# Kernel tuning notes

Hardware: AMD Instinct MI355X
Metric: run time of the kernel (lower is better)

The kernel has to match this reference:

```python
import jax, jax.numpy as jnp
import numpy as np

B, S, E, H = 4, 2048, 512, 8
DH = E // H
EPS = 1e-5

def _ln(x, g, b):
    m = jnp.mean(x, axis=-1, keepdims=True)
    v = jnp.var(x, axis=-1, keepdims=True)
    return (x - m) * jax.lax.rsqrt(v + EPS) * g + b

def setup_inputs() -> dict:
    key = jax.random.key(0)
    ks = jax.random.split(key, 8)
    sc = 0.02
    return {
        "x": jax.random.normal(ks[0], (B, S, E), dtype=jnp.float32),
        "ln1_g": jnp.ones((E,), jnp.float32),
        "ln1_b": jnp.zeros((E,), jnp.float32),
        "in_proj_w": sc * jax.random.normal(ks[1], (3 * E, E), jnp.float32),
        "in_proj_b": jnp.zeros((3 * E,), jnp.float32),
        "out_w": sc * jax.random.normal(ks[2], (E, E), jnp.float32),
        "out_b": jnp.zeros((E,), jnp.float32),
        "ln2_g": jnp.ones((E,), jnp.float32),
        "ln2_b": jnp.zeros((E,), jnp.float32),
        "fc1_w": sc * jax.random.normal(ks[3], (E, E), jnp.float32),
        "fc1_b": jnp.zeros((E,), jnp.float32),
        "fc2_w": sc * jax.random.normal(ks[4], (E, E), jnp.float32),
        "fc2_b": jnp.zeros((E,), jnp.float32),
    }

def reference(x, ln1_g, ln1_b, in_proj_w, in_proj_b, out_w, out_b,
              ln2_g, ln2_b, fc1_w, fc1_b, fc2_w, fc2_b):
    # pre-LN
    z = _ln(x, ln1_g, ln1_b)
    # qkv projection (torch MHA packed in_proj: [3E, E])
    qkv = z @ in_proj_w.T + in_proj_b          # [B,S,3E]
    q, k, v = jnp.split(qkv, 3, axis=-1)
    q = q.reshape(B, S, H, DH)
    k = k.reshape(B, S, H, DH)
    v = v.reshape(B, S, H, DH)
    scores = jnp.einsum("bqhd,bkhd->bhqk", q, k) / np.sqrt(DH).astype(np.float32)
    causal = jnp.triu(jnp.ones((S, S), dtype=bool), k=1)  # True = masked
    neg = jnp.finfo(scores.dtype).min
    scores = jnp.where(causal, neg, scores)
    attn = jax.nn.softmax(scores, axis=-1)      # [B,H,S,S]
    ctx = jnp.einsum("bhqk,bkhd->bqhd", attn, v).reshape(B, S, E)
    attn_out = ctx @ out_w.T + out_b
    # torch MHA with need_weights=True averages over heads by default
    attn_weights = jnp.mean(attn, axis=1)       # [B,S,S]
    z2 = x + attn_out
    y = _ln(z2, ln2_g, ln2_b)
    y = jax.nn.leaky_relu(y @ fc1_w.T + fc1_b, negative_slope=0.01)
    y = y @ fc2_w.T + fc2_b
    y = y + z2
    return (y, attn_weights)
```

## Files before the change

kernel.cpp:

```cpp
#include <hip/hip_runtime.h>

typedef short bf16x8 __attribute__((ext_vector_type(8)));
typedef float f32x4 __attribute__((ext_vector_type(4)));
typedef unsigned short u16x8 __attribute__((ext_vector_type(8)));

#define NB 4
#define SQ 2048
#define EM 512
#define NH 8
#define DHD 64
#define QSCALE 0.1803368801111731f

__device__ __forceinline__ unsigned short f2bf(float x) {
  unsigned u = __float_as_uint(x);
  u += 0x7FFFu + ((u >> 16) & 1u);
  return (unsigned short)(u >> 16);
}

__device__ __forceinline__ int sw8(int row, int col8) { return col8 ^ ((row & 7) << 3); }

__device__ __forceinline__ void glds16(const void* g, void* l) {
  __builtin_amdgcn_global_load_lds(
      (const __attribute__((address_space(1))) void*)g,
      (__attribute__((address_space(3))) void*)l, 16, 0, 0);
}

__global__ __launch_bounds__(256) void f2bf4_kernel(
    const float* __restrict__ w0, const float* __restrict__ w1,
    const float* __restrict__ w2, const float* __restrict__ w3,
    unsigned short* __restrict__ o0, unsigned short* __restrict__ o1,
    unsigned short* __restrict__ o2, unsigned short* __restrict__ o3) {
  int i = (blockIdx.x * 256 + threadIdx.x) * 8;
  const float* src;
  unsigned short* dst;
  int off;
  if (i < 786432) { src = w0; dst = o0; off = i; }
  else if (i < 1048576) { src = w1; dst = o1; off = i - 786432; }
  else if (i < 1310720) { src = w2; dst = o2; off = i - 1048576; }
  else { src = w3; dst = o3; off = i - 1310720; }
  f32x4 a = *(const f32x4*)(src + off);
  f32x4 b = *(const f32x4*)(src + off + 4);
  u16x8 o;
#pragma unroll
  for (int j = 0; j < 4; ++j) { o[j] = f2bf(a[j]); o[j + 4] = f2bf(b[j]); }
  *(u16x8*)(dst + off) = o;
}

__global__ __launch_bounds__(256) void ln_kernel(const float* __restrict__ x,
                                                 const float* __restrict__ g,
                                                 const float* __restrict__ bb,
                                                 unsigned short* __restrict__ out) {
  int tid = threadIdx.x;
  int row = blockIdx.x * 4 + (tid >> 6);
  int lane = tid & 63;
  size_t base = (size_t)row * EM + lane * 8;
  f32x4 v0 = *(const f32x4*)(x + base);
  f32x4 v1 = *(const f32x4*)(x + base + 4);
  float s = 0.f, q = 0.f;
#pragma unroll
  for (int j = 0; j < 4; ++j) { s += v0[j] + v1[j]; q += v0[j] * v0[j] + v1[j] * v1[j]; }
#pragma unroll
  for (int m = 1; m < 64; m <<= 1) { s += __shfl_xor(s, m); q += __shfl_xor(q, m); }
  float mean = s * (1.f / EM);
  float var = q * (1.f / EM) - mean * mean;
  float rs = rsqrtf(var + 1e-5f);
  f32x4 g0 = *(const f32x4*)(g + lane * 8), g1 = *(const f32x4*)(g + lane * 8 + 4);
  f32x4 b0 = *(const f32x4*)(bb + lane * 8), b1 = *(const f32x4*)(bb + lane * 8 + 4);
  u16x8 o;
#pragma unroll
  for (int j = 0; j < 4; ++j) {
    o[j] = f2bf((v0[j] - mean) * rs * g0[j] + b0[j]);
    o[j + 4] = f2bf((v1[j] - mean) * rs * g1[j] + b1[j]);
  }
  *(u16x8*)(out + base) = o;
}

template <bool LEAKY, bool RESID, bool OUTF32, bool QKV>
__global__ __launch_bounds__(256) void gemm64(
    const unsigned short* __restrict__ A, const unsigned short* __restrict__ Bm,
    const float* __restrict__ bias, const float* __restrict__ resid,
    float* __restrict__ outf, unsigned short* __restrict__ outh,
    unsigned short* __restrict__ qo, unsigned short* __restrict__ ko,
    unsigned short* __restrict__ vo, int M, int N, int K) {
  __shared__ unsigned short As[2][64][64];
  __shared__ unsigned short Bs[2][64][64];
  int m0 = blockIdx.x * 64, n0 = blockIdx.y * 64;
  int t = threadIdx.x;
  int wv = t >> 6, ln = t & 63, lg = ln >> 4, lr = ln & 15;
  int rsub = ln >> 3;
  int csw = ((ln & 7) ^ rsub) * 8;
  f32x4 acc[4];
#pragma unroll
  for (int c = 0; c < 4; ++c)
#pragma unroll
    for (int r = 0; r < 4; ++r) acc[c][r] = 0.f;

  const unsigned short* ag0 = A + (size_t)(m0 + wv * 16 + rsub) * K + csw;
  const unsigned short* ag1 = A + (size_t)(m0 + wv * 16 + 8 + rsub) * K + csw;
  const unsigned short* bg0 = Bm + (size_t)(n0 + wv * 16 + rsub) * K + csw;
  const unsigned short* bg1 = Bm + (size_t)(n0 + wv * 16 + 8 + rsub) * K + csw;

  glds16(ag0, &As[0][wv * 16][0]);
  glds16(ag1, &As[0][wv * 16 + 8][0]);
  glds16(bg0, &Bs[0][wv * 16][0]);
  glds16(bg1, &Bs[0][wv * 16 + 8][0]);

  int nk = K >> 6;
  for (int ki = 0; ki < nk; ++ki) {
    int cur = ki & 1;
    __syncthreads();
    if (ki + 1 < nk) {
      int nb = cur ^ 1;
      int ko_ = (ki + 1) * 64;
      glds16(ag0 + ko_, &As[nb][wv * 16][0]);
      glds16(ag1 + ko_, &As[nb][wv * 16 + 8][0]);
      glds16(bg0 + ko_, &Bs[nb][wv * 16][0]);
      glds16(bg1 + ko_, &Bs[nb][wv * 16 + 8][0]);
    }
#pragma unroll
    for (int kk = 0; kk < 64; kk += 32) {
      int arw = wv * 16 + lr;
      bf16x8 af = *(const bf16x8*)&As[cur][arw][sw8(arw, kk + lg * 8)];
#pragma unroll
      for (int c = 0; c < 4; ++c) {
        int brw = c * 16 + lr;
        bf16x8 bf = *(const bf16x8*)&Bs[cur][brw][sw8(brw, kk + lg * 8)];
        acc[c] = __builtin_amdgcn_mfma_f32_16x16x32_bf16(af, bf, acc[c], 0, 0, 0);
      }
    }
  }
#pragma unroll
  for (int c = 0; c < 4; ++c) {
    int C_ = n0 + c * 16 + lr;
    float bv = bias[C_];
#pragma unroll
    for (int r = 0; r < 4; ++r) {
      int R_ = m0 + wv * 16 + lg * 4 + r;
      float v = acc[c][r] + bv;
      if (LEAKY) v = v > 0.f ? v : 0.01f * v;
      if (RESID) v += resid[(size_t)R_ * N + C_];
      if (QKV) {
        int which = C_ >> 9, f = C_ & 511, h = f >> 6, d = f & 63;
        int b_ = R_ >> 11, s_ = R_ & 2047;
        if (which == 0) {
          qo[(((size_t)b_ * NH + h) * SQ + s_) * DHD + d] = f2bf(v * QSCALE);
        } else if (which == 1) {
          ko[(((size_t)b_ * NH + h) * SQ + s_) * DHD + d] = f2bf(v);
        } else {
          vo[(((size_t)b_ * NH + h) * DHD + d) * SQ + s_] = f2bf(v);
        }
      } else if (OUTF32) {
        outf[(size_t)R_ * N + C_] = v;
      } else {
        outh[(size_t)R_ * N + C_] = f2bf(v);
      }
    }
  }
}

template <bool QKV>
__global__ __launch_bounds__(256) void gemm128(
    const unsigned short* __restrict__ A, const unsigned short* __restrict__ Bm,
    const float* __restrict__ bias, unsigned short* __restrict__ qo,
    unsigned short* __restrict__ ko, unsigned short* __restrict__ vo,
    int M, int N, int K) {
  __shared__ unsigned short As[2][128][64];
  __shared__ unsigned short Bs[2][128][64];
  int m0 = blockIdx.x * 128, n0 = blockIdx.y * 128;
  int t = threadIdx.x;
  int wv = t >> 6, ln = t & 63, lg = ln >> 4, lr = ln & 15;
  int wr = wv >> 1, wc = wv & 1;
  int rsub = ln >> 3;
  int csw = ((ln & 7) ^ rsub) * 8;
  f32x4 acc[4][4];
#pragma unroll
  for (int m = 0; m < 4; ++m)
#pragma unroll
    for (int n = 0; n < 4; ++n)
#pragma unroll
      for (int r = 0; r < 4; ++r) acc[m][n][r] = 0.f;

  const unsigned short* agb = A + (size_t)(m0 + wv * 8 + rsub) * K + csw;
  const unsigned short* bgb = Bm + (size_t)(n0 + wv * 8 + rsub) * K + csw;

#pragma unroll
  for (int i = 0; i < 4; ++i) {
    glds16(agb + (size_t)(i * 32) * K, &As[0][i * 32 + wv * 8][0]);
    glds16(bgb + (size_t)(i * 32) * K, &Bs[0][i * 32 + wv * 8][0]);
  }

  int nk = K >> 6;
  for (int ki = 0; ki < nk; ++ki) {
    int cur = ki & 1;
    __syncthreads();
    if (ki + 1 < nk) {
      int nb = cur ^ 1;
      int ko_ = (ki + 1) * 64;
#pragma unroll
      for (int i = 0; i < 4; ++i) {
        glds16(agb + (size_t)(i * 32) * K + ko_, &As[nb][i * 32 + wv * 8][0]);
        glds16(bgb + (size_t)(i * 32) * K + ko_, &Bs[nb][i * 32 + wv * 8][0]);
      }
    }
#pragma unroll
    for (int kk = 0; kk < 64; kk += 32) {
      bf16x8 af[4], bfr[4];
#pragma unroll
      for (int m = 0; m < 4; ++m) {
        int arw = wr * 64 + m * 16 + lr;
        af[m] = *(const bf16x8*)&As[cur][arw][sw8(arw, kk + lg * 8)];
      }
#pragma unroll
      for (int n = 0; n < 4; ++n) {
        int brw = wc * 64 + n * 16 + lr;
        bfr[n] = *(const bf16x8*)&Bs[cur][brw][sw8(brw, kk + lg * 8)];
      }
#pragma unroll
      for (int m = 0; m < 4; ++m)
#pragma unroll
        for (int n = 0; n < 4; ++n)
          acc[m][n] = __builtin_amdgcn_mfma_f32_16x16x32_bf16(af[m], bfr[n], acc[m][n], 0, 0, 0);
    }
  }

#pragma unroll
  for (int n = 0; n < 4; ++n) {
    int C_ = n0 + wc * 64 + n * 16 + lr;
    float bv = bias[C_];
#pragma unroll
    for (int m = 0; m < 4; ++m) {
#pragma unroll
      for (int r = 0; r < 4; ++r) {
        int R_ = m0 + wr * 64 + m * 16 + lg * 4 + r;
        float v = acc[m][n][r] + bv;
        int which = C_ >> 9, f = C_ & 511, h = f >> 6, d = f & 63;
        int b_ = R_ >> 11, s_ = R_ & 2047;
        if (which == 0) {
          qo[(((size_t)b_ * NH + h) * SQ + s_) * DHD + d] = f2bf(v * QSCALE);
        } else if (which == 1) {
          ko[(((size_t)b_ * NH + h) * SQ + s_) * DHD + d] = f2bf(v);
        } else {
          vo[(((size_t)b_ * NH + h) * DHD + d) * SQ + s_] = f2bf(v);
        }
      }
    }
  }
}

__global__ __launch_bounds__(256) void flash_kernel(
    const unsigned short* __restrict__ Q, const unsigned short* __restrict__ Kb,
    const unsigned short* __restrict__ Vt, unsigned short* __restrict__ ctx,
    float* __restrict__ mstat, float* __restrict__ lstat) {
  __shared__ unsigned short Ks[2][64][64];
  __shared__ unsigned short Vs[2][64][64];
  __shared__ unsigned short Ps[4][16][64];
  int h = blockIdx.y, b = blockIdx.z;
  int t = threadIdx.x, wv = t >> 6, ln = t & 63, lg = ln >> 4, lr = ln & 15;
  int rsub = ln >> 3;
  int csw = ((ln & 7) ^ rsub) * 8;
  size_t headoff = ((size_t)b * NH + h) * SQ;
  const unsigned short* kg0 = Kb + (headoff + wv * 16 + rsub) * DHD + csw;
  const unsigned short* kg1 = Kb + (headoff + wv * 16 + 8 + rsub) * DHD + csw;
  const unsigned short* vg0 = Vt + (((size_t)b * NH + h) * DHD + wv * 16 + rsub) * SQ + csw;
  const unsigned short* vg1 = Vt + (((size_t)b * NH + h) * DHD + wv * 16 + 8 + rsub) * SQ + csw;

  bf16x8 vones;
#pragma unroll
  for (int j = 0; j < 8; ++j) vones[j] = (lr == 0) ? (short)0x3F80 : (short)0;

  for (int half = 0; half < 2; ++half) {
    int qt = half ? blockIdx.x : (31 - blockIdx.x);
    int qb = qt * 64;
    const unsigned short* qrow = Q + (headoff + qb + wv * 16 + lr) * DHD;
    bf16x8 aq0 = *(const bf16x8*)(qrow + lg * 8);
    bf16x8 aq1 = *(const bf16x8*)(qrow + 32 + lg * 8);

    f32x4 cacc[4], lacc;
#pragma unroll
    for (int nd = 0; nd < 4; ++nd)
#pragma unroll
      for (int r = 0; r < 4; ++r) cacc[nd][r] = 0.f;
#pragma unroll
    for (int r = 0; r < 4; ++r) lacc[r] = 0.f;
    float mrun[4];
#pragma unroll
    for (int r = 0; r < 4; ++r) mrun[r] = -__builtin_inff();

    int nkt = qt + 1;
    __syncthreads();
    glds16(kg0, &Ks[0][wv * 16][0]);
    glds16(kg1, &Ks[0][wv * 16 + 8][0]);
    glds16(vg0, &Vs[0][wv * 16][0]);
    glds16(vg1, &Vs[0][wv * 16 + 8][0]);

    for (int kt = 0; kt < nkt; ++kt) {
      int cur = kt & 1;
      __syncthreads();
      if (kt + 1 < nkt) {
        int nb = cur ^ 1;
        size_t ko_ = (size_t)(kt + 1) * 64;
        glds16(kg0 + ko_ * DHD, &Ks[nb][wv * 16][0]);
        glds16(kg1 + ko_ * DHD, &Ks[nb][wv * 16 + 8][0]);
        glds16(vg0 + ko_, &Vs[nb][wv * 16][0]);
        glds16(vg1 + ko_, &Vs[nb][wv * 16 + 8][0]);
      }

      float sv[4][4];
      __builtin_amdgcn_s_setprio(1);
#pragma unroll
      for (int nt = 0; nt < 4; ++nt) {
        f32x4 sf;
#pragma unroll
        for (int r = 0; r < 4; ++r) sf[r] = 0.f;
        int brw = nt * 16 + lr;
        bf16x8 bk0 = *(const bf16x8*)&Ks[cur][brw][sw8(brw, lg * 8)];
        bf16x8 bk1 = *(const bf16x8*)&Ks[cur][brw][sw8(brw, 32 + lg * 8)];
        sf = __builtin_amdgcn_mfma_f32_16x16x32_bf16(aq0, bk0, sf, 0, 0, 0);
        sf = __builtin_amdgcn_mfma_f32_16x16x32_bf16(aq1, bk1, sf, 0, 0, 0);
#pragma unroll
        for (int r = 0; r < 4; ++r) sv[nt][r] = sf[r];
      }
      __builtin_amdgcn_s_setprio(0);
      if (kt == nkt - 1) {
        int kbase = kt * 64;
#pragma unroll
        for (int nt = 0; nt < 4; ++nt) {
          int kcol = kbase + nt * 16 + lr;
#pragma unroll
          for (int r = 0; r < 4; ++r) {
            int qr = qb + wv * 16 + lg * 4 + r;
            if (kcol > qr) sv[nt][r] = -__builtin_inff();
          }
        }
      }

      float lmax[4];
      bool need = false;
#pragma unroll
      for (int r = 0; r < 4; ++r) {
        lmax[r] = fmaxf(fmaxf(sv[0][r], sv[1][r]), fmaxf(sv[2][r], sv[3][r]));
        need |= (lmax[r] > mrun[r] + 8.f);
      }
      if (__any(need)) {
#pragma unroll
        for (int r = 0; r < 4; ++r) {
          float tm = lmax[r];
#pragma unroll
          for (int m = 1; m < 16; m <<= 1) tm = fmaxf(tm, __shfl_xor(tm, m));
          float mn = fmaxf(mrun[r], tm);
          float sc = exp2f(mrun[r] - mn);
          mrun[r] = mn;
          lacc[r] *= sc;
#pragma unroll
          for (int nd = 0; nd < 4; ++nd) cacc[nd][r] *= sc;
        }
      }
#pragma unroll
      for (int r = 0; r < 4; ++r) {
        int prow = lg * 4 + r;
#pragma unroll
        for (int nt = 0; nt < 4; ++nt) {
          float p = exp2f(sv[nt][r] - mrun[r]);
          Ps[wv][prow][sw8(prow, nt * 16 + lr)] =
              (unsigned short)(__float_as_uint(p) >> 16);
        }
      }

      bf16x8 pf0 = *(const bf16x8*)&Ps[wv][lr][sw8(lr, lg * 8)];
      bf16x8 pf1 = *(const bf16x8*)&Ps[wv][lr][sw8(lr, 32 + lg * 8)];
      __builtin_amdgcn_s_setprio(1);
      lacc = __builtin_amdgcn_mfma_f32_16x16x32_bf16(pf0, vones, lacc, 0, 0, 0);
      lacc = __builtin_amdgcn_mfma_f32_16x16x32_bf16(pf1, vones, lacc, 0, 0, 0);
#pragma unroll
      for (int nd = 0; nd < 4; ++nd) {
        int vrw = nd * 16 + lr;
        bf16x8 vf0 = *(const bf16x8*)&Vs[cur][vrw][sw8(vrw, lg * 8)];
        bf16x8 vf1 = *(const bf16x8*)&Vs[cur][vrw][sw8(vrw, 32 + lg * 8)];
        cacc[nd] = __builtin_amdgcn_mfma_f32_16x16x32_bf16(pf0, vf0, cacc[nd], 0, 0, 0);
        cacc[nd] = __builtin_amdgcn_mfma_f32_16x16x32_bf16(pf1, vf1, cacc[nd], 0, 0, 0);
      }
      __builtin_amdgcn_s_setprio(0);
    }

    float inv[4];
#pragma unroll
    for (int r = 0; r < 4; ++r) inv[r] = 1.f / __shfl(lacc[r], ln & 48);
#pragma unroll
    for (int nd = 0; nd < 4; ++nd)
#pragma unroll
      for (int r = 0; r < 4; ++r) {
        size_t dst = ((size_t)b * SQ + qb + wv * 16 + lg * 4 + r) * EM + h * DHD + nd * 16 + lr;
        ctx[dst] = f2bf(cacc[nd][r] * inv[r]);
      }
    if (lr == 0) {
#pragma unroll
      for (int r = 0; r < 4; ++r) {
        int row = qb + wv * 16 + lg * 4 + r;
        mstat[headoff + row] = mrun[r];
        lstat[headoff + row] = 0.125f * inv[r];
      }
    }
  }
}

__global__ __launch_bounds__(256) void attnw_kernel(
    const unsigned short* __restrict__ Q, const unsigned short* __restrict__ Kb,
    const float* __restrict__ mstat, const float* __restrict__ lstat,
    float* __restrict__ aw) {
  int kt2 = blockIdx.x, qt = blockIdx.y, b = blockIdx.z;
  int qb = qt * 64, kb = kt2 * 128;
  int t = threadIdx.x;
  float* tile = aw + ((size_t)b * SQ + qb) * SQ + kb;
  if (2 * kt2 > qt) {
    int row = t >> 2, cbase = (t & 3) * 32;
    f32x4 z;
#pragma unroll
    for (int j = 0; j < 4; ++j) z[j] = 0.f;
    float* p = tile + (size_t)row * SQ + cbase;
#pragma unroll
    for (int j = 0; j < 8; ++j) *(f32x4*)(p + j * 4) = z;
    return;
  }
  __shared__ unsigned short Ks[2][2][64][64];
  int wv = t >> 6, ln = t & 63, lg = ln >> 4, lr = ln & 15;
  int rsub = ln >> 3;
  int csw = ((ln & 7) ^ rsub) * 8;
  size_t khstride = (size_t)SQ * DHD;
  const unsigned short* kg00 = Kb + (((size_t)b * NH) * SQ + kb + wv * 16 + rsub) * DHD + csw;
  const unsigned short* kg01 = kg00 + (size_t)8 * DHD;
  const unsigned short* kg10 = kg00 + (size_t)64 * DHD;
  const unsigned short* kg11 = kg00 + (size_t)72 * DHD;
  const unsigned short* qg = Q + (((size_t)b * NH) * SQ + qb + wv * 16 + lr) * DHD + lg * 8;
  size_t mbase = (size_t)b * NH * SQ + qb + wv * 16 + lg * 4;

  glds16(kg00, &Ks[0][0][wv * 16][0]);
  glds16(kg01, &Ks[0][0][wv * 16 + 8][0]);
  glds16(kg10, &Ks[0][1][wv * 16][0]);
  glds16(kg11, &Ks[0][1][wv * 16 + 8][0]);

  bf16x8 aqc0 = *(const bf16x8*)qg;
  bf16x8 aqc1 = *(const bf16x8*)(qg + 32);
  bf16x8 aqn0 = *(const bf16x8*)(qg + khstride);
  bf16x8 aqn1 = *(const bf16x8*)(qg + khstride + 32);
  float mmc[4], lic[4], mmn[4], lin[4];
#pragma unroll
  for (int r = 0; r < 4; ++r) {
    mmc[r] = mstat[mbase + r];
    lic[r] = lstat[mbase + r];
    mmn[r] = mstat[mbase + SQ + r];
    lin[r] = lstat[mbase + SQ + r];
  }

  f32x4 facc[2][4];
#pragma unroll
  for (int j = 0; j < 2; ++j)
#pragma unroll
    for (int nt = 0; nt < 4; ++nt)
#pragma unroll
      for (int r = 0; r < 4; ++r) facc[j][nt][r] = 0.f;

  for (int h = 0; h < NH; ++h) {
    int cur = h & 1;
    __syncthreads();
    if (h + 1 < NH) {
      size_t ho = (size_t)(h + 1) * khstride;
      glds16(kg00 + ho, &Ks[cur ^ 1][0][wv * 16][0]);
      glds16(kg01 + ho, &Ks[cur ^ 1][0][wv * 16 + 8][0]);
      glds16(kg10 + ho, &Ks[cur ^ 1][1][wv * 16][0]);
      glds16(kg11 + ho, &Ks[cur ^ 1][1][wv * 16 + 8][0]);
    }

#pragma unroll
    for (int nt = 0; nt < 4; ++nt) {
      int brw = nt * 16 + lr;
      f32x4 sf0, sf1;
#pragma unroll
      for (int r = 0; r < 4; ++r) { sf0[r] = 0.f; sf1[r] = 0.f; }
      bf16x8 bk00 = *(const bf16x8*)&Ks[cur][0][brw][sw8(brw, lg * 8)];
      bf16x8 bk01 = *(const bf16x8*)&Ks[cur][0][brw][sw8(brw, 32 + lg * 8)];
      bf16x8 bk10 = *(const bf16x8*)&Ks[cur][1][brw][sw8(brw, lg * 8)];
      bf16x8 bk11 = *(const bf16x8*)&Ks[cur][1][brw][sw8(brw, 32 + lg * 8)];
      sf0 = __builtin_amdgcn_mfma_f32_16x16x32_bf16(aqc0, bk00, sf0, 0, 0, 0);
      sf1 = __builtin_amdgcn_mfma_f32_16x16x32_bf16(aqc0, bk10, sf1, 0, 0, 0);
      sf0 = __builtin_amdgcn_mfma_f32_16x16x32_bf16(aqc1, bk01, sf0, 0, 0, 0);
      sf1 = __builtin_amdgcn_mfma_f32_16x16x32_bf16(aqc1, bk11, sf1, 0, 0, 0);
#pragma unroll
      for (int r = 0; r < 4; ++r) {
        facc[0][nt][r] += exp2f(sf0[r] - mmc[r]) * lic[r];
        facc[1][nt][r] += exp2f(sf1[r] - mmc[r]) * lic[r];
      }
    }

    aqc0 = aqn0; aqc1 = aqn1;
#pragma unroll
    for (int r = 0; r < 4; ++r) { mmc[r] = mmn[r]; lic[r] = lin[r]; }
    if (h + 2 < NH) {
      aqn0 = *(const bf16x8*)(qg + (size_t)(h + 2) * khstride);
      aqn1 = *(const bf16x8*)(qg + (size_t)(h + 2) * khstride + 32);
#pragma unroll
      for (int r = 0; r < 4; ++r) {
        mmn[r] = mstat[mbase + (size_t)(h + 2) * SQ + r];
        lin[r] = lstat[mbase + (size_t)(h + 2) * SQ + r];
      }
    }
  }

#pragma unroll
  for (int j = 0; j < 2; ++j) {
    int ktj = 2 * kt2 + j;
    bool fullmask = (ktj > qt);
    bool dg = (ktj == qt);
#pragma unroll
    for (int nt = 0; nt < 4; ++nt) {
      int kc = kb + j * 64 + nt * 16 + lr;
#pragma unroll
      for (int r = 0; r < 4; ++r) {
        int qr = qb + wv * 16 + lg * 4 + r;
        float v = (fullmask || (dg && kc > qr)) ? 0.f : facc[j][nt][r];
        tile[(size_t)(wv * 16 + lg * 4 + r) * SQ + j * 64 + nt * 16 + lr] = v;
      }
    }
  }
}

extern "C" void kernel_launch(void* const* d_in, const int* in_sizes, int n_in,
                              void* d_out, int out_size, void* d_ws, size_t ws_size,
                              hipStream_t stream) {
  (void)in_sizes; (void)n_in; (void)out_size; (void)ws_size;
  const float* x = (const float*)d_in[0];
  const float* ln1g = (const float*)d_in[1];
  const float* ln1b = (const float*)d_in[2];
  const float* wqkv = (const float*)d_in[3];
  const float* bqkv = (const float*)d_in[4];
  const float* wout = (const float*)d_in[5];
  const float* bout = (const float*)d_in[6];
  const float* ln2g = (const float*)d_in[7];
  const float* ln2b = (const float*)d_in[8];
  const float* wfc1 = (const float*)d_in[9];
  const float* bfc1 = (const float*)d_in[10];
  const float* wfc2 = (const float*)d_in[11];
  const float* bfc2 = (const float*)d_in[12];

  char* ws = (char*)d_ws;
  unsigned short* zctx = (unsigned short*)(ws);
  unsigned short* qb_ = (unsigned short*)(ws + 8388608);
  unsigned short* kb_ = (unsigned short*)(ws + 16777216);
  unsigned short* vb_ = (unsigned short*)(ws + 25165824);
  float* z2 = (float*)(ws + 33554432);
  float* mstat = (float*)(ws + 50331648);
  float* lstat = (float*)(ws + 50593792);
  unsigned short* wqkv_h = (unsigned short*)(ws + 50855936);
  unsigned short* wout_h = (unsigned short*)(ws + 52428800);
  unsigned short* wfc1_h = (unsigned short*)(ws + 52953088);
  unsigned short* wfc2_h = (unsigned short*)(ws + 53477376);
  unsigned short* y1 = qb_;
  unsigned short* h1 = kb_;

  float* outy = (float*)d_out;
  float* outw = outy + (size_t)NB * SQ * EM;

  f2bf4_kernel<<<768, 256, 0, stream>>>(wqkv, wout, wfc1, wfc2,
                                        wqkv_h, wout_h, wfc1_h, wfc2_h);

  ln_kernel<<<2048, 256, 0, stream>>>(x, ln1g, ln1b, zctx);
  gemm128<true><<<dim3(64, 12), 256, 0, stream>>>(
      zctx, wqkv_h, bqkv, qb_, kb_, vb_, 8192, 1536, 512);
  flash_kernel<<<dim3(16, 8, 4), 256, 0, stream>>>(qb_, kb_, vb_, zctx, mstat, lstat);
  attnw_kernel<<<dim3(16, 32, 4), 256, 0, stream>>>(qb_, kb_, mstat, lstat, outw);
  gemm64<false, true, true, false><<<dim3(128, 8), 256, 0, stream>>>(
      zctx, wout_h, bout, x, z2, nullptr, nullptr, nullptr, nullptr, 8192, 512, 512);
  ln_kernel<<<2048, 256, 0, stream>>>(z2, ln2g, ln2b, y1);
  gemm64<true, false, false, false><<<dim3(128, 8), 256, 0, stream>>>(
      y1, wfc1_h, bfc1, nullptr, nullptr, h1, nullptr, nullptr, nullptr, 8192, 512, 512);
  gemm64<false, true, true, false><<<dim3(128, 8), 256, 0, stream>>>(
      h1, wfc2_h, bfc2, z2, outy, nullptr, nullptr, nullptr, nullptr, 8192, 512, 512);
}
```

Baseline: 186.2 us.

## Widen flash attention key tiles from 64 to 128 keys per iteration

After: 184.8 us. About the same (-0.8%).

```diff
diff --git a/kernel.cpp b/kernel.cpp
--- a/kernel.cpp
+++ b/kernel.cpp
@@ -18,6 +18,7 @@
 }
 
 __device__ __forceinline__ int sw8(int row, int col8) { return col8 ^ ((row & 7) << 3); }
+__device__ __forceinline__ int sw16(int row, int col8) { return col8 ^ ((row & 15) << 3); }
 
 __device__ __forceinline__ void glds16(const void* g, void* l) {
   __builtin_amdgcn_global_load_lds(
@@ -251,18 +252,21 @@
     const unsigned short* __restrict__ Q, const unsigned short* __restrict__ Kb,
     const unsigned short* __restrict__ Vt, unsigned short* __restrict__ ctx,
     float* __restrict__ mstat, float* __restrict__ lstat) {
-  __shared__ unsigned short Ks[2][64][64];
-  __shared__ unsigned short Vs[2][64][64];
-  __shared__ unsigned short Ps[4][16][64];
+  __shared__ unsigned short Ks[2][128][64];
+  __shared__ unsigned short Vs[2][64][128];
+  __shared__ unsigned short Ps[4][16][128];
   int h = blockIdx.y, b = blockIdx.z;
   int t = threadIdx.x, wv = t >> 6, ln = t & 63, lg = ln >> 4, lr = ln & 15;
-  int rsub = ln >> 3;
-  int csw = ((ln & 7) ^ rsub) * 8;
   size_t headoff = ((size_t)b * NH + h) * SQ;
-  const unsigned short* kg0 = Kb + (headoff + wv * 16 + rsub) * DHD + csw;
-  const unsigned short* kg1 = Kb + (headoff + wv * 16 + 8 + rsub) * DHD + csw;
-  const unsigned short* vg0 = Vt + (((size_t)b * NH + h) * DHD + wv * 16 + rsub) * SQ + csw;
-  const unsigned short* vg1 = Vt + (((size_t)b * NH + h) * DHD + wv * 16 + 8 + rsub) * SQ + csw;
+  size_t vbase = ((size_t)b * NH + h) * DHD;
+
+  int cswK = ((ln & 7) ^ (ln >> 3)) * 8;
+  const unsigned short* kgb = Kb + (headoff + wv * 32 + (ln >> 3)) * DHD + cswK;
+  int vrow4 = ln >> 4;
+  const unsigned short* vgb = Vt + (vbase + wv * 16 + vrow4) * SQ;
+  int vcsw[4];
+#pragma unroll
+  for (int g = 0; g < 4; ++g) vcsw[g] = ((ln & 15) ^ (g * 4 + vrow4)) * 8;
 
   bf16x8 vones;
 #pragma unroll
@@ -286,29 +290,32 @@
 #pragma unroll
     for (int r = 0; r < 4; ++r) mrun[r] = -__builtin_inff();
 
-    int nkt = qt + 1;
+    int nkt = (qt + 2) >> 1;
     __syncthreads();
-    glds16(kg0, &Ks[0][wv * 16][0]);
-    glds16(kg1, &Ks[0][wv * 16 + 8][0]);
-    glds16(vg0, &Vs[0][wv * 16][0]);
-    glds16(vg1, &Vs[0][wv * 16 + 8][0]);
+#pragma unroll
+    for (int g = 0; g < 4; ++g) {
+      glds16(kgb + (size_t)(g * 8) * DHD, &Ks[0][wv * 32 + g * 8][0]);
+      glds16(vgb + (size_t)(g * 4) * SQ + vcsw[g], &Vs[0][wv * 16 + g * 4][0]);
+    }
 
     for (int kt = 0; kt < nkt; ++kt) {
       int cur = kt & 1;
+      int kb = kt * 128;
       __syncthreads();
       if (kt + 1 < nkt) {
         int nb = cur ^ 1;
-        size_t ko_ = (size_t)(kt + 1) * 64;
-        glds16(kg0 + ko_ * DHD, &Ks[nb][wv * 16][0]);
-        glds16(kg1 + ko_ * DHD, &Ks[nb][wv * 16 + 8][0]);
-        glds16(vg0 + ko_, &Vs[nb][wv * 16][0]);
-        glds16(vg1 + ko_, &Vs[nb][wv * 16 + 8][0]);
-      }
-
-      float sv[4][4];
+        size_t ko_ = (size_t)(kt + 1) * 128;
+#pragma unroll
+        for (int g = 0; g < 4; ++g) {
+          glds16(kgb + (ko_ + g * 8) * DHD, &Ks[nb][wv * 32 + g * 8][0]);
+          glds16(vgb + (size_t)(g * 4) * SQ + ko_ + vcsw[g], &Vs[nb][wv * 16 + g * 4][0]);
+        }
+      }
+
+      float sv[8][4];
       __builtin_amdgcn_s_setprio(1);
 #pragma unroll
-      for (int nt = 0; nt < 4; ++nt) {
+      for (int nt = 0; nt < 8; ++nt) {
         f32x4 sf;
 #pragma unroll
         for (int r = 0; r < 4; ++r) sf[r] = 0.f;
@@ -322,10 +329,9 @@
       }
       __builtin_amdgcn_s_setprio(0);
       if (kt == nkt - 1) {
-        int kbase = kt * 64;
-#pragma unroll
-        for (int nt = 0; nt < 4; ++nt) {
-          int kcol = kbase + nt * 16 + lr;
+#pragma unroll
+        for (int nt = 0; nt < 8; ++nt) {
+          int kcol = kb + nt * 16 + lr;
 #pragma unroll
           for (int r = 0; r < 4; ++r) {
             int qr = qb + wv * 16 + lg * 4 + r;
@@ -338,7 +344,9 @@
       bool need = false;
 #pragma unroll
       for (int r = 0; r < 4; ++r) {
-        lmax[r] = fmaxf(fmaxf(sv[0][r], sv[1][r]), fmaxf(sv[2][r], sv[3][r]));
+        float m0_ = fmaxf(fmaxf(sv[0][r], sv[1][r]), fmaxf(sv[2][r], sv[3][r]));
+        float m1_ = fmaxf(fmaxf(sv[4][r], sv[5][r]), fmaxf(sv[6][r], sv[7][r]));
+        lmax[r] = fmaxf(m0_, m1_);
         need |= (lmax[r] > mrun[r] + 8.f);
       }
       if (__any(need)) {
@@ -358,26 +366,31 @@
 #pragma unroll
       for (int r = 0; r < 4; ++r) {
         int prow = lg * 4 + r;
-#pragma unroll
-        for (int nt = 0; nt < 4; ++nt) {
+        int rx = (prow & 15) << 3;
+#pragma unroll
+        for (int nt = 0; nt < 8; ++nt) {
           float p = exp2f(sv[nt][r] - mrun[r]);
-          Ps[wv][prow][sw8(prow, nt * 16 + lr)] =
+          Ps[wv][prow][(nt * 16 + lr) ^ rx] =
               (unsigned short)(__float_as_uint(p) >> 16);
         }
       }
 
-      bf16x8 pf0 = *(const bf16x8*)&Ps[wv][lr][sw8(lr, lg * 8)];
-      bf16x8 pf1 = *(const bf16x8*)&Ps[wv][lr][sw8(lr, 32 + lg * 8)];
+      bf16x8 pf[4];
+#pragma unroll
+      for (int ks = 0; ks < 4; ++ks)
+        pf[ks] = *(const bf16x8*)&Ps[wv][lr][sw16(lr, ks * 32 + lg * 8)];
       __builtin_amdgcn_s_setprio(1);
-      lacc = __builtin_amdgcn_mfma_f32_16x16x32_bf16(pf0, vones, lacc, 0, 0, 0);
-      lacc = __builtin_amdgcn_mfma_f32_16x16x32_bf16(pf1, vones, lacc, 0, 0, 0);
+#pragma unroll
+      for (int ks = 0; ks < 4; ++ks)
+        lacc = __builtin_amdgcn_mfma_f32_16x16x32_bf16(pf[ks], vones, lacc, 0, 0, 0);
 #pragma unroll
       for (int nd = 0; nd < 4; ++nd) {
         int vrw = nd * 16 + lr;
-        bf16x8 vf0 = *(const bf16x8*)&Vs[cur][vrw][sw8(vrw, lg * 8)];
-        bf16x8 vf1 = *(const bf16x8*)&Vs[cur][vrw][sw8(vrw, 32 + lg * 8)];
-        cacc[nd] = __builtin_amdgcn_mfma_f32_16x16x32_bf16(pf0, vf0, cacc[nd], 0, 0, 0);
-        cacc[nd] = __builtin_amdgcn_mfma_f32_16x16x32_bf16(pf1, vf1, cacc[nd], 0, 0, 0);
+#pragma unroll
+        for (int ks = 0; ks < 4; ++ks) {
+          bf16x8 vf = *(const bf16x8*)&Vs[cur][vrw][sw16(vrw, ks * 32 + lg * 8)];
+          cacc[nd] = __builtin_amdgcn_mfma_f32_16x16x32_bf16(pf[ks], vf, cacc[nd], 0, 0, 0);
+        }
       }
       __builtin_amdgcn_s_setprio(0);
     }
```
